# Optimization experiments

Hardware: AMD Instinct MI355X
Metric: run time of the kernel (lower is better)

The kernel has to match this reference:

```python
import jax, jax.numpy as jnp
import numpy as np

B, L, E, H = 128, 256, 256, 512


def setup_inputs() -> dict:
    key = jax.random.key(0)
    ks = jax.random.split(key, 16)
    s = 0.02
    return {
        "embedded_inputs": jax.random.normal(ks[0], (B, L, E), jnp.float32),
        "decoder_input": jax.random.normal(ks[1], (B, E), jnp.float32),
        "dec_h": jax.random.normal(ks[2], (B, H), jnp.float32),
        "dec_c": jax.random.normal(ks[3], (B, H), jnp.float32),
        "context": jax.random.normal(ks[4], (B, L, H), jnp.float32),
        # Decoder params
        "W_i2h": jax.random.normal(ks[5], (4 * H, E), jnp.float32) * s,
        "b_i2h": jnp.zeros((4 * H,), jnp.float32),
        "W_h2h": jax.random.normal(ks[6], (4 * H, H), jnp.float32) * s,
        "b_h2h": jnp.zeros((4 * H,), jnp.float32),
        "W_out": jax.random.normal(ks[7], (H, 2 * H), jnp.float32) * s,
        "b_out": jnp.zeros((H,), jnp.float32),
        # Attention params
        "W_inp": jax.random.normal(ks[8], (H, H), jnp.float32) * s,
        "b_inp": jnp.zeros((H,), jnp.float32),
        "W_ctx": jax.random.normal(ks[9], (H, H), jnp.float32) * s,  # Conv1d(k=1) kernel squeezed
        "b_ctx": jnp.zeros((H,), jnp.float32),
        "V": jax.random.uniform(ks[10], (H,), jnp.float32, -1.0, 1.0),
    }


def reference(embedded_inputs, decoder_input, dec_h, dec_c, context,
              W_i2h, b_i2h, W_h2h, b_h2h, W_out, b_out,
              W_inp, b_inp, W_ctx, b_ctx, V):
    # Precompute projected context: Conv1d(k=1) == per-position linear. ctx: [B, H, L]
    ctx = jnp.einsum("blh,gh->bgl", context, W_ctx) + b_ctx[None, :, None]
    seq_len = embedded_inputs.shape[1]

    def step(carry, _):
        x, h, c, mask = carry
        gates = x @ W_i2h.T + b_i2h + h @ W_h2h.T + b_h2h
        i, f, g, o = jnp.split(gates, 4, axis=1)
        c_t = jax.nn.sigmoid(f) * c + jax.nn.sigmoid(i) * jnp.tanh(g)
        h_t = jax.nn.sigmoid(o) * jnp.tanh(c_t)
        # attention
        inp = h_t @ W_inp.T + b_inp                              # [B, H]
        scores = jnp.einsum("h,bhl->bl", V, jnp.tanh(inp[:, :, None] + ctx))
        att = jnp.where(mask == 0, -jnp.inf, scores)
        alpha = jax.nn.softmax(att, axis=-1)                     # [B, L]
        hidden = jnp.einsum("bhl,bl->bh", ctx, alpha)
        h_new = jnp.tanh(jnp.concatenate([hidden, h_t], axis=1) @ W_out.T + b_out)
        # pointer selection
        idx = jnp.argmax(alpha * mask, axis=1)                   # [B]
        one_hot = jax.nn.one_hot(idx, seq_len, dtype=mask.dtype)
        mask_new = mask * (1.0 - one_hot)
        next_x = jnp.take_along_axis(embedded_inputs, idx[:, None, None], axis=1)[:, 0, :]
        return (next_x, h_new, c_t, mask_new), (alpha, idx)

    mask0 = jnp.ones((embedded_inputs.shape[0], seq_len), jnp.float32)
    (x_f, h_f, c_f, _), (alphas, ptrs) = jax.lax.scan(
        step, (decoder_input, dec_h, dec_c, mask0), None, length=seq_len)
    outputs = jnp.transpose(alphas, (1, 0, 2))   # [B, L, L]
    pointers = jnp.transpose(ptrs, (1, 0))       # [B, L]
    return outputs, pointers, h_f, c_f
```

## Files before the change

kernel.cpp:

```cpp
#include <hip/hip_runtime.h>

#define B 128
#define L 256
#define E 256
#define H 512
#define NBLK 256
#define NTHR 512

typedef float f4 __attribute__((ext_vector_type(4)));

#define WS_CTX 0u
#define WS_HT  18874368u
#define WS_HH  18939904u
#define WS_HID 19005440u
#define WS_INP 19071232u
#define WS_XT  19136768u
#define WS_FLG 19169536u

#define OUT_ALPHA 0u
#define OUT_PTR   8388608u
#define OUT_H     8421376u
#define OUT_C     8486912u

#define L2E 1.4426950408889634f

__device__ __forceinline__ float fast_rcp(float x) { return __builtin_amdgcn_rcpf(x); }

__device__ __forceinline__ float ftanh(float x) {
  float e = exp2f(x * (2.0f * L2E));
  return 1.0f - 2.0f * fast_rcp(e + 1.0f);
}
__device__ __forceinline__ float fsig(float x) {
  float e = exp2f(-x * L2E);
  return fast_rcp(1.0f + e);
}

#define CLD1(v0, p0)                                                          \
  asm volatile("global_load_dwordx4 %0, %1, off sc0 sc1\n\t"                  \
               "s_waitcnt vmcnt(0)"                                           \
               : "=&v"(v0) : "v"(p0) : "memory")

#define CLD2(va, pa)                                                          \
  asm volatile("global_load_dwordx4 %0, %2, off sc0 sc1\n\t"                  \
               "global_load_dwordx4 %1, %3, off sc0 sc1\n\t"                  \
               "s_waitcnt vmcnt(0)"                                           \
               : "=&v"(va[0]), "=&v"(va[1])                                   \
               : "v"(pa[0]), "v"(pa[1]) : "memory")

#define CLD4(va, pa)                                                          \
  asm volatile("global_load_dwordx4 %0, %4, off sc0 sc1\n\t"                  \
               "global_load_dwordx4 %1, %5, off sc0 sc1\n\t"                  \
               "global_load_dwordx4 %2, %6, off sc0 sc1\n\t"                  \
               "global_load_dwordx4 %3, %7, off sc0 sc1\n\t"                  \
               "s_waitcnt vmcnt(0)"                                           \
               : "=&v"(va[0]), "=&v"(va[1]), "=&v"(va[2]), "=&v"(va[3])       \
               : "v"(pa[0]), "v"(pa[1]), "v"(pa[2]), "v"(pa[3]) : "memory")

#define CLD6(va, pa)                                                          \
  asm volatile("global_load_dwordx4 %0, %6, off sc0 sc1\n\t"                  \
               "global_load_dwordx4 %1, %7, off sc0 sc1\n\t"                  \
               "global_load_dwordx4 %2, %8, off sc0 sc1\n\t"                  \
               "global_load_dwordx4 %3, %9, off sc0 sc1\n\t"                  \
               "global_load_dwordx4 %4, %10, off sc0 sc1\n\t"                 \
               "global_load_dwordx4 %5, %11, off sc0 sc1\n\t"                 \
               "s_waitcnt vmcnt(0)"                                           \
               : "=&v"(va[0]), "=&v"(va[1]), "=&v"(va[2]), "=&v"(va[3]),      \
                 "=&v"(va[4]), "=&v"(va[5])                                   \
               : "v"(pa[0]), "v"(pa[1]), "v"(pa[2]), "v"(pa[3]),              \
                 "v"(pa[4]), "v"(pa[5]) : "memory")

#define CST4_1(p0, v0)                                                        \
  asm volatile("global_store_dwordx4 %0, %1, off sc0 sc1\n\t"                 \
               "s_waitcnt expcnt(0)"                                          \
               :: "v"(p0), "v"(v0) : "memory")

__device__ __forceinline__ void gbar(unsigned* flags, unsigned tgt) {
  asm volatile("s_waitcnt vmcnt(0) lgkmcnt(0) expcnt(0)" ::: "memory");
  __syncthreads();
  if (threadIdx.x == 0) {
    unsigned* p = flags + blockIdx.x;
    asm volatile("global_store_dword %0, %1, off sc0 sc1" :: "v"(p), "v"(tgt) : "memory");
  }
  if (blockIdx.x == 0) {
    if (threadIdx.x < 64) {
      const unsigned* fp = flags + threadIdx.x * 4;
      for (;;) {
        unsigned f0, f1, f2, f3;
        asm volatile("global_load_dwordx4 v[20:23], %4, off sc0 sc1\n\t"
                     "s_waitcnt vmcnt(0)\n\t"
                     "v_mov_b32 %0, v20\n\t"
                     "v_mov_b32 %1, v21\n\t"
                     "v_mov_b32 %2, v22\n\t"
                     "v_mov_b32 %3, v23"
                     : "=v"(f0), "=v"(f1), "=v"(f2), "=v"(f3)
                     : "v"(fp) : "memory", "v20", "v21", "v22", "v23");
        bool ok = (f0 >= tgt) && (f1 >= tgt) && (f2 >= tgt) && (f3 >= tgt);
        if (__all(ok)) break;
        __builtin_amdgcn_s_sleep(1);
      }
    }
    __syncthreads();
    if (threadIdx.x == 0) {
      unsigned* gp = flags + 320;
      asm volatile("global_store_dword %0, %1, off sc0 sc1" :: "v"(gp), "v"(tgt) : "memory");
    }
  } else {
    if (threadIdx.x == 0) {
      const unsigned* gp = flags + 320;
      for (;;) {
        unsigned g;
        asm volatile("global_load_dword %0, %1, off sc0 sc1\n\ts_waitcnt vmcnt(0)"
                     : "=&v"(g) : "v"(gp) : "memory");
        if (g >= tgt) break;
        __builtin_amdgcn_s_sleep(4);
      }
    }
  }
  __syncthreads();
}

__global__ __launch_bounds__(256) void k_ctx(const float* __restrict__ context,
                                             const float* __restrict__ Wc,
                                             const float* __restrict__ bc,
                                             float* __restrict__ ws) {
  __shared__ float a_lds[64][33];
  __shared__ float b_lds[32][68];
  int t = threadIdx.x;
  int m0 = blockIdx.x * 64;
  int n0 = blockIdx.y * 64;
  int tx = t & 15, ty = t >> 4;
  float acc[4][4] = {};
  for (int kc = 0; kc < 16; ++kc) {
    int k0 = kc * 32;
    __syncthreads();
#pragma unroll
    for (int i = 0; i < 2; ++i) {
      int f40 = t + i * 256;
      int mm = f40 >> 3;
      int k4 = (f40 & 7) * 4;
      float4 v = *(const float4*)&context[(size_t)(m0 + mm) * H + k0 + k4];
      a_lds[mm][k4] = v.x; a_lds[mm][k4 + 1] = v.y; a_lds[mm][k4 + 2] = v.z; a_lds[mm][k4 + 3] = v.w;
    }
#pragma unroll
    for (int i = 0; i < 2; ++i) {
      int f40 = t + i * 256;
      int nn = f40 >> 3;
      int k4 = (f40 & 7) * 4;
      float4 v = *(const float4*)&Wc[(size_t)(n0 + nn) * H + k0 + k4];
      b_lds[k4][nn] = v.x; b_lds[k4 + 1][nn] = v.y; b_lds[k4 + 2][nn] = v.z; b_lds[k4 + 3][nn] = v.w;
    }
    __syncthreads();
#pragma unroll
    for (int kk = 0; kk < 32; ++kk) {
      float4 bv = *(const float4*)&b_lds[kk][tx * 4];
      float a0 = a_lds[ty * 4 + 0][kk], a1 = a_lds[ty * 4 + 1][kk];
      float a2 = a_lds[ty * 4 + 2][kk], a3 = a_lds[ty * 4 + 3][kk];
      acc[0][0] += a0 * bv.x; acc[0][1] += a0 * bv.y; acc[0][2] += a0 * bv.z; acc[0][3] += a0 * bv.w;
      acc[1][0] += a1 * bv.x; acc[1][1] += a1 * bv.y; acc[1][2] += a1 * bv.z; acc[1][3] += a1 * bv.w;
      acc[2][0] += a2 * bv.x; acc[2][1] += a2 * bv.y; acc[2][2] += a2 * bv.z; acc[2][3] += a2 * bv.w;
      acc[3][0] += a3 * bv.x; acc[3][1] += a3 * bv.y; acc[3][2] += a3 * bv.z; acc[3][3] += a3 * bv.w;
    }
  }
  float b0v = bc[n0 + tx * 4], b1v = bc[n0 + tx * 4 + 1], b2v = bc[n0 + tx * 4 + 2], b3v = bc[n0 + tx * 4 + 3];
#pragma unroll
  for (int i = 0; i < 4; ++i) {
    size_t o = WS_CTX + (size_t)(m0 + ty * 4 + i) * H + n0 + tx * 4;
    float4 v; v.x = acc[i][0] + b0v; v.y = acc[i][1] + b1v; v.z = acc[i][2] + b2v; v.w = acc[i][3] + b3v;
    *(float4*)&ws[o] = v;
  }
}

__global__ __launch_bounds__(256) void k_init(const float* __restrict__ dec_h,
                                              const float* __restrict__ dec_in,
                                              float* __restrict__ ws) {
  int flat = blockIdx.x * 256 + threadIdx.x;
  if (flat < 65536) {
    ws[WS_HH + flat] = dec_h[flat];
  } else if (flat < 98304) {
    ws[WS_XT + (flat - 65536)] = dec_in[flat - 65536];
  } else if (flat < 98816) {
    ((unsigned*)(ws + WS_FLG))[flat - 98304] = 0u;
  }
}

__global__ __launch_bounds__(512, 1) void k_main(
    const float* __restrict__ Wi2h, const float* __restrict__ bi2h,
    const float* __restrict__ Wh2h, const float* __restrict__ bh2h,
    const float* __restrict__ Wout, const float* __restrict__ bout,
    const float* __restrict__ Winp, const float* __restrict__ binp,
    const float* __restrict__ Vv,   const float* __restrict__ emb,
    const float* __restrict__ dec_c,
    float* __restrict__ ws,         float* __restrict__ out) {
  __shared__ float s_act[13504];
  __shared__ float s_maskP[256];
  __shared__ float s_mw[8], s_dw[8];
  __shared__ float s_red[4];
  __shared__ int   s_redi[4];
  __shared__ int   s_wc[4], s_wb[4];
  __shared__ int   s_mi, s_cnt;

  unsigned* flags = (unsigned*)(ws + WS_FLG);
  const int bid = blockIdx.x;
  const int t = threadIdx.x;
  const int wv = t >> 6, ln = t & 63;
  unsigned tgt = 0;

  float creg = 0.f;

  if (bid < 128 && t < 256) s_maskP[t] = 1.0f;
  __syncthreads();

  for (int step = 0; step < L; ++step) {
    {
      const int jt = bid >> 3, bt = bid & 7;
      const int u0 = jt * 16, b0 = bt * 16;
      float* sact = s_act;
      float* sg   = s_act + 12352;
      f4 va[6]; const float* pa[6]; int sb[6], sq[6];
#pragma unroll
      for (int it = 0; it < 6; ++it) {
        unsigned c = (unsigned)(t + it * 512);
        int bl = (int)(c / 192u);
        int kq = (int)(c - (unsigned)bl * 192u);
        int kg = kq * 4;
        sb[it] = bl; sq[it] = kq;
        pa[it] = (kg < 256) ? ws + WS_XT + (size_t)(b0 + bl) * 256 + kg
                            : ws + WS_HH + (size_t)(b0 + bl) * 512 + (kg - 256);
      }
      CLD6(va, pa);
      __builtin_amdgcn_sched_barrier(0);
#pragma unroll
      for (int it = 0; it < 6; ++it) *(f4*)&sact[sb[it] * 772 + sq[it] * 4] = va[it];
      __syncthreads();

      const int jj = t >> 4, bb = t & 15;
      const int g = jj >> 3, up = (jj & 7) * 2;
      const int r0 = g * 512 + u0 + up;
      float a0 = 0.f, a1 = 0.f;
      {
        const float* w0 = Wi2h + (size_t)r0 * 256;
        const float* w1 = w0 + 256;
        const float* sa = sact + bb * 772;
#pragma unroll 8
        for (int k4 = 0; k4 < 64; ++k4) {
          float4 x = *(const float4*)&sa[k4 * 4];
          float4 p = *(const float4*)&w0[k4 * 4];
          float4 q = *(const float4*)&w1[k4 * 4];
          a0 += p.x * x.x + p.y * x.y + p.z * x.z + p.w * x.w;
          a1 += q.x * x.x + q.y * x.y + q.z * x.z + q.w * x.w;
        }
        const float* v0 = Wh2h + (size_t)r0 * 512;
        const float* v1 = v0 + 512;
        const float* shh = sa + 256;
#pragma unroll 8
        for (int k4 = 0; k4 < 128; ++k4) {
          float4 x = *(const float4*)&shh[k4 * 4];
          float4 p = *(const float4*)&v0[k4 * 4];
          float4 q = *(const float4*)&v1[k4 * 4];
          a0 += p.x * x.x + p.y * x.y + p.z * x.z + p.w * x.w;
          a1 += q.x * x.x + q.y * x.y + q.z * x.z + q.w * x.w;
        }
      }
      sg[(g * 16 + up) * 17 + bb]     = a0;
      sg[(g * 16 + up + 1) * 17 + bb] = a1;
      __syncthreads();
      if (t < 256) {
        const int uu = t >> 4, b2 = t & 15;
        const int j0 = u0 + uu;
        float si_ = sg[(     uu) * 17 + b2] + bi2h[       j0] + bh2h[       j0];
        float sf_ = sg[(16 + uu) * 17 + b2] + bi2h[ 512 + j0] + bh2h[ 512 + j0];
        float sg_ = sg[(32 + uu) * 17 + b2] + bi2h[1024 + j0] + bh2h[1024 + j0];
        float so_ = sg[(48 + uu) * 17 + b2] + bi2h[1536 + j0] + bh2h[1536 + j0];
        if (step == 0) creg = dec_c[(size_t)(b0 + b2) * 512 + j0];
        float cn = fsig(sf_) * creg + fsig(si_) * ftanh(sg_);
        creg = cn;
        float htv = fsig(so_) * ftanh(cn);
        s_act[b2 * 17 + uu] = htv;
        if (step == L - 1) out[OUT_C + (size_t)(b0 + b2) * 512 + j0] = cn;
      }
      __syncthreads();
      if (t < 64) {
        const int b2 = t >> 2, q = t & 3;
        f4 hv;
        hv[0] = s_act[b2 * 17 + q * 4 + 0];
        hv[1] = s_act[b2 * 17 + q * 4 + 1];
        hv[2] = s_act[b2 * 17 + q * 4 + 2];
        hv[3] = s_act[b2 * 17 + q * 4 + 3];
        float* hp = ws + WS_HT + (size_t)(b0 + b2) * 512 + u0 + q * 4;
        CST4_1(hp, hv);
      }
    }
    ++tgt; gbar(flags, tgt);

    {
      const int gt = bid >> 4, bt = bid & 15;
      const int g0 = gt * 32, b0 = bt * 8;
      float* si = s_act;
      float* stmp = s_act + 4128;
      f4 va[2]; const float* pa[2];
#pragma unroll
      for (int it = 0; it < 2; ++it) {
        int c = t + it * 512;
        int bl = c >> 7, kq = c & 127;
        pa[it] = ws + WS_HT + (size_t)(b0 + bl) * 512 + kq * 4;
      }
      CLD2(va, pa);
      __builtin_amdgcn_sched_barrier(0);
#pragma unroll
      for (int it = 0; it < 2; ++it) {
        int c = t + it * 512;
        int bl = c >> 7, kq = c & 127;
        *(f4*)&si[bl * 516 + kq * 4] = va[it];
      }
      __syncthreads();
      if (t < 256) {
        const int gl = t >> 3, bb = t & 7;
        const float* w = Winp + (size_t)(g0 + gl) * 512;
        const float* sa = si + bb * 516;
        float acc = 0.f;
#pragma unroll 8
        for (int k4 = 0; k4 < 128; ++k4) {
          float4 ww = *(const float4*)&w[k4 * 4];
          float4 xx = *(const float4*)&sa[k4 * 4];
          acc += ww.x * xx.x + ww.y * xx.y + ww.z * xx.z + ww.w * xx.w;
        }
        stmp[bb * 33 + gl] = acc + binp[g0 + gl];
      }
      __syncthreads();
      if (t < 64) {
        const int bb = t >> 3, q = t & 7;
        f4 v;
        v[0] = stmp[bb * 33 + q * 4 + 0];
        v[1] = stmp[bb * 33 + q * 4 + 1];
        v[2] = stmp[bb * 33 + q * 4 + 2];
        v[3] = stmp[bb * 33 + q * 4 + 3];
        float* p = ws + WS_INP + (size_t)(b0 + bb) * 512 + g0 + q * 4;
        CST4_1(p, v);
      }
    }
    ++tgt; gbar(flags, tgt);

    if (bid < 128) {
      const int b = bid;
      float* s_inp  = s_act;
      float* s_sc   = s_act + 512;
      int*   s_li   = (int*)(s_act + 768);
      float* s_hidp = s_act + 1024;
      float* s_out  = s_act + 5120;
      if (t < 128) {
        f4 v;
        const float* p = ws + WS_INP + (size_t)b * 512 + t * 4;
        CLD1(v, p);
        *(f4*)&s_inp[t * 4] = v;
      }
      __syncthreads();
      const int d0 = ln * 8;
      float inp8[8], v8[8];
#pragma unroll
      for (int i = 0; i < 8; ++i) { inp8[i] = s_inp[d0 + i]; v8[i] = Vv[d0 + i]; }
      bool validl = (t < 256) && (s_maskP[t] != 0.f);
      unsigned long long bal = __ballot(validl);
      if (t < 256 && (t & 63) == 0) s_wc[t >> 6] = (int)__popcll(bal);
      __syncthreads();
      if (t == 0) {
        int base = 0;
#pragma unroll
        for (int i = 0; i < 4; ++i) { s_wb[i] = base; base += s_wc[i]; }
        s_cnt = base;
      }
      __syncthreads();
      if (validl) {
        int idx = s_wb[t >> 6] + (int)__popcll(bal & ((1ull << (t & 63)) - 1ull));
        s_li[idx] = t;
      }
      __syncthreads();
      const int cnt = s_cnt;
      float m = -INFINITY, den = 0.f;
      float hid[8] = {0, 0, 0, 0, 0, 0, 0, 0};
      {
        int slot = wv;
        int l = 0; f4 c0 = {0, 0, 0, 0}, c1 = c0;
        if (slot < cnt) {
          l = s_li[slot];
          const float* cp = ws + WS_CTX + ((size_t)(b * 256 + l) * 512) + d0;
          c0 = *(const f4*)cp; c1 = *(const f4*)(cp + 4);
        }
        while (slot < cnt) {
          const int nslot = slot + 8;
          int nl = 0; f4 n0 = {0, 0, 0, 0}, n1 = n0;
          if (nslot < cnt) {
            nl = s_li[nslot];
            const float* np = ws + WS_CTX + ((size_t)(b * 256 + nl) * 512) + d0;
            n0 = *(const f4*)np; n1 = *(const f4*)(np + 4);
          }
          float part = v8[0] * ftanh(inp8[0] + c0[0]) + v8[1] * ftanh(inp8[1] + c0[1])
                     + v8[2] * ftanh(inp8[2] + c0[2]) + v8[3] * ftanh(inp8[3] + c0[3])
                     + v8[4] * ftanh(inp8[4] + c1[0]) + v8[5] * ftanh(inp8[5] + c1[1])
                     + v8[6] * ftanh(inp8[6] + c1[2]) + v8[7] * ftanh(inp8[7] + c1[3]);
#pragma unroll
          for (int off = 32; off > 0; off >>= 1) part += __shfl_xor(part, off);
          if (ln == 0) s_sc[l] = part;
          float mn = fmaxf(m, part);
          float scale = exp2f((m - mn) * L2E);
          float e = exp2f((part - mn) * L2E);
          den = den * scale + e;
          hid[0] = hid[0] * scale + e * c0[0]; hid[1] = hid[1] * scale + e * c0[1];
          hid[2] = hid[2] * scale + e * c0[2]; hid[3] = hid[3] * scale + e * c0[3];
          hid[4] = hid[4] * scale + e * c1[0]; hid[5] = hid[5] * scale + e * c1[1];
          hid[6] = hid[6] * scale + e * c1[2]; hid[7] = hid[7] * scale + e * c1[3];
          m = mn;
          c0 = n0; c1 = n1; l = nl; slot = nslot;
        }
      }
      if (ln == 0) { s_mw[wv] = m; s_dw[wv] = den; }
      __syncthreads();
      float M = s_mw[0];
#pragma unroll
      for (int w = 1; w < 8; ++w) M = fmaxf(M, s_mw[w]);
      float D = 0.f;
#pragma unroll
      for (int w = 0; w < 8; ++w) D += s_dw[w] * exp2f((s_mw[w] - M) * L2E);
      float fac = exp2f((m - M) * L2E);
#pragma unroll
      for (int i = 0; i < 8; ++i) s_hidp[wv * 512 + d0 + i] = hid[i] * fac;
      __syncthreads();
      const float rD = 1.0f / D;
      {
        float hs = 0.f;
#pragma unroll
        for (int w = 0; w < 8; ++w) hs += s_hidp[w * 512 + t];
        s_out[t] = hs * rD;
      }
      float sc = 0.f; bool valid = false;
      if (t < 256) {
        valid = (s_maskP[t] != 0.f);
        sc = s_sc[t];
        float alpha = valid ? exp2f((sc - M) * L2E) * rD : 0.f;
        out[OUT_ALPHA + ((size_t)b * 256 + step) * 256 + t] = alpha;
        float bs = valid ? sc : -INFINITY;
        int bi = t;
#pragma unroll
        for (int off = 32; off > 0; off >>= 1) {
          float os = __shfl_down(bs, off);
          int oi = __shfl_down(bi, off);
          if (os > bs || (os == bs && oi < bi)) { bs = os; bi = oi; }
        }
        if ((t & 63) == 0) { s_red[t >> 6] = bs; s_redi[t >> 6] = bi; }
      }
      __syncthreads();
      if (t == 0) {
        float mm = s_red[0]; int mi = s_redi[0];
#pragma unroll
        for (int w = 1; w < 4; ++w) {
          if (s_red[w] > mm || (s_red[w] == mm && s_redi[w] < mi)) { mm = s_red[w]; mi = s_redi[w]; }
        }
        s_mi = mi;
      }
      __syncthreads();
      const int mi = s_mi;
      if (t < 128) {
        f4 hv = *(const f4*)&s_out[t * 4];
        float* hp = ws + WS_HID + (size_t)b * 512 + t * 4;
        CST4_1(hp, hv);
      }
      if (t < 64) {
        float4 xv = *(const float4*)&emb[((size_t)b * 256 + mi) * 256 + t * 4];
        f4 xq; xq[0] = xv.x; xq[1] = xv.y; xq[2] = xv.z; xq[3] = xv.w;
        float* xp = ws + WS_XT + (size_t)b * 256 + t * 4;
        CST4_1(xp, xq);
      }
      if (t == 0) {
        out[OUT_PTR + (size_t)b * 256 + step] = (float)mi;
        s_maskP[mi] = 0.f;
      }
    }
    ++tgt; gbar(flags, tgt);

    {
      const int rt = bid >> 4, bt = bid & 15;
      const int r0 = rt * 32, b0 = bt * 8;
      float* sh = s_act;
      float* stmp = s_act + 8224;
      f4 va[4]; const float* pa[4];
#pragma unroll
      for (int it = 0; it < 4; ++it) {
        int c = t + it * 512;
        int bl = c >> 8, kq = c & 255;
        int kg = kq * 4;
        pa[it] = (kg < 512) ? ws + WS_HID + (size_t)(b0 + bl) * 512 + kg
                            : ws + WS_HT + (size_t)(b0 + bl) * 512 + (kg - 512);
      }
      CLD4(va, pa);
      __builtin_amdgcn_sched_barrier(0);
#pragma unroll
      for (int it = 0; it < 4; ++it) {
        int c = t + it * 512;
        int bl = c >> 8, kq = c & 255;
        *(f4*)&sh[bl * 1028 + kq * 4] = va[it];
      }
      __syncthreads();
      if (t < 256) {
        const int rl = t >> 3, bb = t & 7;
        const float* w = Wout + (size_t)(r0 + rl) * 1024;
        const float* sa = sh + bb * 1028;
        float acc = 0.f;
#pragma unroll 8
        for (int k4 = 0; k4 < 256; ++k4) {
          float4 ww = *(const float4*)&w[k4 * 4];
          float4 xx = *(const float4*)&sa[k4 * 4];
          acc += ww.x * xx.x + ww.y * xx.y + ww.z * xx.z + ww.w * xx.w;
        }
        float h = ftanh(acc + bout[r0 + rl]);
        stmp[bb * 33 + rl] = h;
        if (step == L - 1) out[OUT_H + (size_t)(b0 + bb) * 512 + r0 + rl] = h;
      }
      __syncthreads();
      if (t < 64) {
        const int bb = t >> 3, q = t & 7;
        f4 v;
        v[0] = stmp[bb * 33 + q * 4 + 0];
        v[1] = stmp[bb * 33 + q * 4 + 1];
        v[2] = stmp[bb * 33 + q * 4 + 2];
        v[3] = stmp[bb * 33 + q * 4 + 3];
        float* p = ws + WS_HH + (size_t)(b0 + bb) * 512 + r0 + q * 4;
        CST4_1(p, v);
      }
    }
    ++tgt; gbar(flags, tgt);
  }
}

extern "C" void kernel_launch(void* const* d_in, const int* in_sizes, int n_in,
                              void* d_out, int out_size, void* d_ws, size_t ws_size,
                              hipStream_t stream) {
  (void)in_sizes; (void)n_in; (void)out_size; (void)ws_size;
  const float* emb    = (const float*)d_in[0];
  const float* dec_in = (const float*)d_in[1];
  const float* dec_h  = (const float*)d_in[2];
  const float* dec_c  = (const float*)d_in[3];
  const float* ctx_in = (const float*)d_in[4];
  const float* W_i2h  = (const float*)d_in[5];
  const float* b_i2h  = (const float*)d_in[6];
  const float* W_h2h  = (const float*)d_in[7];
  const float* b_h2h  = (const float*)d_in[8];
  const float* W_out  = (const float*)d_in[9];
  const float* b_out  = (const float*)d_in[10];
  const float* W_inp  = (const float*)d_in[11];
  const float* b_inp  = (const float*)d_in[12];
  const float* W_ctx  = (const float*)d_in[13];
  const float* b_ctx  = (const float*)d_in[14];
  const float* Vv     = (const float*)d_in[15];
  float* out = (float*)d_out;
  float* ws  = (float*)d_ws;

  k_ctx<<<dim3(512, 8), 256, 0, stream>>>(ctx_in, W_ctx, b_ctx, ws);
  k_init<<<386, 256, 0, stream>>>(dec_h, dec_in, ws);
  k_main<<<NBLK, NTHR, 0, stream>>>(W_i2h, b_i2h, W_h2h, b_h2h, W_out, b_out,
                                    W_inp, b_inp, Vv, emb, dec_c, ws, out);
}
```

Baseline: 18.97 ms.

## Fuse attention input projection into attention phase, drop one grid barrier per step

```diff
diff --git a/kernel.cpp b/kernel.cpp
--- a/kernel.cpp
+++ b/kernel.cpp
@@ -13,7 +13,6 @@
 #define WS_HT  18874368u
 #define WS_HH  18939904u
 #define WS_HID 19005440u
-#define WS_INP 19071232u
 #define WS_XT  19136768u
 #define WS_FLG 19169536u
 
@@ -39,13 +38,6 @@
   asm volatile("global_load_dwordx4 %0, %1, off sc0 sc1\n\t"                  \
                "s_waitcnt vmcnt(0)"                                           \
                : "=&v"(v0) : "v"(p0) : "memory")
-
-#define CLD2(va, pa)                                                          \
-  asm volatile("global_load_dwordx4 %0, %2, off sc0 sc1\n\t"                  \
-               "global_load_dwordx4 %1, %3, off sc0 sc1\n\t"                  \
-               "s_waitcnt vmcnt(0)"                                           \
-               : "=&v"(va[0]), "=&v"(va[1])                                   \
-               : "v"(pa[0]), "v"(pa[1]) : "memory")
 
 #define CLD4(va, pa)                                                          \
   asm volatile("global_load_dwordx4 %0, %4, off sc0 sc1\n\t"                  \
@@ -212,7 +204,8 @@
 
   for (int step = 0; step < L; ++step) {
     {
-      const int jt = bid >> 3, bt = bid & 7;
+      const int jt = (bid & 7) * 4 + ((bid >> 3) & 3);
+      const int bt = bid >> 5;
       const int u0 = jt * 16, b0 = bt * 16;
       float* sact = s_act;
       float* sg   = s_act + 12352;
@@ -292,54 +285,6 @@
     }
     ++tgt; gbar(flags, tgt);
 
-    {
-      const int gt = bid >> 4, bt = bid & 15;
-      const int g0 = gt * 32, b0 = bt * 8;
-      float* si = s_act;
-      float* stmp = s_act + 4128;
-      f4 va[2]; const float* pa[2];
-#pragma unroll
-      for (int it = 0; it < 2; ++it) {
-        int c = t + it * 512;
-        int bl = c >> 7, kq = c & 127;
-        pa[it] = ws + WS_HT + (size_t)(b0 + bl) * 512 + kq * 4;
-      }
-      CLD2(va, pa);
-      __builtin_amdgcn_sched_barrier(0);
-#pragma unroll
-      for (int it = 0; it < 2; ++it) {
-        int c = t + it * 512;
-        int bl = c >> 7, kq = c & 127;
-        *(f4*)&si[bl * 516 + kq * 4] = va[it];
-      }
-      __syncthreads();
-      if (t < 256) {
-        const int gl = t >> 3, bb = t & 7;
-        const float* w = Winp + (size_t)(g0 + gl) * 512;
-        const float* sa = si + bb * 516;
-        float acc = 0.f;
-#pragma unroll 8
-        for (int k4 = 0; k4 < 128; ++k4) {
-          float4 ww = *(const float4*)&w[k4 * 4];
-          float4 xx = *(const float4*)&sa[k4 * 4];
-          acc += ww.x * xx.x + ww.y * xx.y + ww.z * xx.z + ww.w * xx.w;
-        }
-        stmp[bb * 33 + gl] = acc + binp[g0 + gl];
-      }
-      __syncthreads();
-      if (t < 64) {
-        const int bb = t >> 3, q = t & 7;
-        f4 v;
-        v[0] = stmp[bb * 33 + q * 4 + 0];
-        v[1] = stmp[bb * 33 + q * 4 + 1];
-        v[2] = stmp[bb * 33 + q * 4 + 2];
-        v[3] = stmp[bb * 33 + q * 4 + 3];
-        float* p = ws + WS_INP + (size_t)(b0 + bb) * 512 + g0 + q * 4;
-        CST4_1(p, v);
-      }
-    }
-    ++tgt; gbar(flags, tgt);
-
     if (bid < 128) {
       const int b = bid;
       float* s_inp  = s_act;
@@ -347,11 +292,24 @@
       int*   s_li   = (int*)(s_act + 768);
       float* s_hidp = s_act + 1024;
       float* s_out  = s_act + 5120;
+      float* s_ht   = s_act + 5632;
       if (t < 128) {
         f4 v;
-        const float* p = ws + WS_INP + (size_t)b * 512 + t * 4;
+        const float* p = ws + WS_HT + (size_t)b * 512 + t * 4;
         CLD1(v, p);
-        *(f4*)&s_inp[t * 4] = v;
+        *(f4*)&s_ht[t * 4] = v;
+      }
+      __syncthreads();
+      {
+        const float* w = Winp + (size_t)t * 512;
+        float acc = 0.f;
+#pragma unroll 8
+        for (int k4 = 0; k4 < 128; ++k4) {
+          float4 ww = *(const float4*)&w[k4 * 4];
+          float4 xx = *(const float4*)&s_ht[k4 * 4];
+          acc += ww.x * xx.x + ww.y * xx.y + ww.z * xx.z + ww.w * xx.w;
+        }
+        s_inp[t] = acc + binp[t];
       }
       __syncthreads();
       const int d0 = ln * 8;
@@ -382,16 +340,18 @@
         int l = 0; f4 c0 = {0, 0, 0, 0}, c1 = c0;
         if (slot < cnt) {
           l = s_li[slot];
-          const float* cp = ws + WS_CTX + ((size_t)(b * 256 + l) * 512) + d0;
-          c0 = *(const f4*)cp; c1 = *(const f4*)(cp + 4);
+          const f4* cp = (const f4*)(ws + WS_CTX + ((size_t)(b * 256 + l) * 512) + d0);
+          c0 = __builtin_nontemporal_load(cp);
+          c1 = __builtin_nontemporal_load(cp + 1);
         }
         while (slot < cnt) {
           const int nslot = slot + 8;
           int nl = 0; f4 n0 = {0, 0, 0, 0}, n1 = n0;
           if (nslot < cnt) {
             nl = s_li[nslot];
-            const float* np = ws + WS_CTX + ((size_t)(b * 256 + nl) * 512) + d0;
-            n0 = *(const f4*)np; n1 = *(const f4*)(np + 4);
+            const f4* np = (const f4*)(ws + WS_CTX + ((size_t)(b * 256 + nl) * 512) + d0);
+            n0 = __builtin_nontemporal_load(np);
+            n1 = __builtin_nontemporal_load(np + 1);
           }
           float part = v8[0] * ftanh(inp8[0] + c0[0]) + v8[1] * ftanh(inp8[1] + c0[1])
                      + v8[2] * ftanh(inp8[2] + c0[2]) + v8[3] * ftanh(inp8[3] + c0[3])
@@ -477,7 +437,8 @@
     ++tgt; gbar(flags, tgt);
 
     {
-      const int rt = bid >> 4, bt = bid & 15;
+      const int rt = (bid & 7) * 2 + ((bid >> 3) & 1);
+      const int bt = bid >> 4;
       const int r0 = rt * 32, b0 = bt * 8;
       float* sh = s_act;
       float* stmp = s_act + 8224;
```

Measured after the change: 23.24 ms. +22.5%, slower.
